# Performance work log

Measured on AMD Instinct MI355X. Metric: run time of the kernel, lower is better.

The kernel has to match this reference:

```python
import jax, jax.numpy as jnp
import numpy as np

SPLIT_PARAM = [4, 4, 4, 4]   # split sizes along h; sum == H
EPS = 1e-6                   # GeM clamp epsilon
NUM_SEGMENTS = 32            # number of packed sequences (B)


def setup_inputs() -> dict:
    key = jax.random.key(0)
    k1, k2 = jax.random.split(key)
    B, S, C, O, H, Wd = NUM_SEGMENTS, 4096, 128, 256, 16, 11
    x = jax.random.normal(k1, (1, C, S, H, Wd), dtype=jnp.float32)
    # ragged lengths: B positive ints summing exactly to S
    rng = np.random.default_rng(0)
    cuts = np.sort(rng.choice(np.arange(1, S), B - 1, replace=False))
    seqL = jnp.asarray(np.diff(np.concatenate([[0], cuts, [S]])), dtype=jnp.int32)
    W = jax.random.normal(k2, (O, C), dtype=jnp.float32) * 0.05  # 1x1 conv weight, bias=False
    p = jnp.ones((len(SPLIT_PARAM),), dtype=jnp.float32) * 6.5   # per-part GeM power
    return {"x": x, "seqL": seqL, "W": W, "p": p}


def reference(x, seqL, W, p):
    # x: [1, C, S, H, W] frames packed along dim 2; seqL: [B] lengths, sum == S
    _, C, S, H, Wd = x.shape
    # map each frame to its sequence id (ragged segment boundaries)
    bounds = jnp.cumsum(seqL)
    seg_ids = jnp.searchsorted(bounds, jnp.arange(S), side='right')  # [S]
    xs = jnp.transpose(x[0], (1, 0, 2, 3))                           # [S, C, H, W]
    pooled = jax.ops.segment_max(xs, seg_ids, num_segments=NUM_SEGMENTS)  # [B, C, H, W]
    # BasicConv2d: 1x1 conv, stride 1, no padding, no bias
    y = jnp.einsum('bchw,oc->bohw', pooled, W)                       # [B, O, H, W]
    # split along h and apply GeM (bin_num=[1]) with per-part power p[i]
    feats = []
    start = 0
    for i, sp in enumerate(SPLIT_PARAM):
        part = y[:, :, start:start + sp, :].reshape(y.shape[0], y.shape[1], -1)  # [B, O, sp*W]
        g = jnp.mean(jnp.clip(part, EPS, None) ** p[i], axis=-1) ** (1.0 / p[i])  # [B, O]
        feats.append(g[..., None])
        start += sp
    return jnp.concatenate(feats, -1)  # [B, O, m]
```

## Files before the change

kernel.cpp:

```cpp
#include <hip/hip_runtime.h>
#include <cmath>

#define C_DIM 128
#define S_DIM 4096
#define HW    176
#define B_SEG 32
#define O_DIM 256

__global__ __launch_bounds__(192) void seg_max_kernel(
    const float* __restrict__ x, const int* __restrict__ seqL,
    float* __restrict__ pooled)
{
    int bc = blockIdx.x;
    int c  = bc & (C_DIM - 1);
    int b  = bc >> 7;

    int s0 = 0;
    for (int i = 0; i < b; ++i) s0 += seqL[i];
    int len = seqL[b];

    int e = threadIdx.x;
    if (e >= HW) return;

    const float* xp = x + ((size_t)c * S_DIM + s0) * HW + e;
    float m = -INFINITY;
    int s = 0;
    for (; s + 4 <= len; s += 4) {
        float a0 = xp[(size_t)(s + 0) * HW];
        float a1 = xp[(size_t)(s + 1) * HW];
        float a2 = xp[(size_t)(s + 2) * HW];
        float a3 = xp[(size_t)(s + 3) * HW];
        m = fmaxf(m, fmaxf(fmaxf(a0, a1), fmaxf(a2, a3)));
    }
    for (; s < len; ++s) m = fmaxf(m, xp[(size_t)s * HW]);

    pooled[((size_t)b * C_DIM + c) * HW + e] = m;
}

__global__ __launch_bounds__(128) void conv_gem_kernel(
    const float* __restrict__ pooled, const float* __restrict__ Wm,
    const float* __restrict__ p, float* __restrict__ out)
{
    int bx = blockIdx.x;
    int b  = bx >> 3;
    int ot = bx & 7;
    int t  = threadIdx.x;
    int o_l  = t & 31;
    int part = t >> 5;
    int o = ot * 32 + o_l;

    __shared__ __align__(16) float pl[32 * HW];
    __shared__ float wl[32 * 33];

    float acc[44];
#pragma unroll
    for (int j = 0; j < 44; ++j) acc[j] = 0.f;

    for (int c0 = 0; c0 < C_DIM; c0 += 32) {
        __syncthreads();
        const float* src = pooled + ((size_t)b * C_DIM + c0) * HW;
        for (int i = t; i < 32 * HW; i += 128) pl[i] = src[i];
        for (int i = t; i < 32 * 32; i += 128) {
            int oo = i >> 5;
            int cc = i & 31;
            wl[cc * 33 + oo] = Wm[(size_t)(ot * 32 + oo) * C_DIM + c0 + cc];
        }
        __syncthreads();

        float wreg[32];
#pragma unroll
        for (int cc = 0; cc < 32; ++cc) wreg[cc] = wl[cc * 33 + o_l];

#pragma unroll 4
        for (int cc = 0; cc < 32; ++cc) {
            const float4* p4 = (const float4*)(pl + cc * HW + part * 44);
            float w = wreg[cc];
#pragma unroll
            for (int j = 0; j < 11; ++j) {
                float4 v = p4[j];
                acc[4 * j + 0] = fmaf(v.x, w, acc[4 * j + 0]);
                acc[4 * j + 1] = fmaf(v.y, w, acc[4 * j + 1]);
                acc[4 * j + 2] = fmaf(v.z, w, acc[4 * j + 2]);
                acc[4 * j + 3] = fmaf(v.w, w, acc[4 * j + 3]);
            }
        }
    }

    float pw = p[part];
    float s = 0.f;
#pragma unroll
    for (int j = 0; j < 44; ++j) {
        float v = fmaxf(acc[j], 1e-6f);
        s += __expf(pw * __logf(v));
    }
    float g = __powf(s * (1.0f / 44.0f), 1.0f / pw);
    out[((size_t)b * O_DIM + o) * 4 + part] = g;
}

extern "C" void kernel_launch(void* const* d_in, const int* in_sizes, int n_in,
                              void* d_out, int out_size, void* d_ws, size_t ws_size,
                              hipStream_t stream)
{
    const float* x    = (const float*)d_in[0];
    const int*   seqL = (const int*)d_in[1];
    const float* Wm   = (const float*)d_in[2];
    const float* p    = (const float*)d_in[3];
    float* out    = (float*)d_out;
    float* pooled = (float*)d_ws;

    seg_max_kernel<<<B_SEG * C_DIM, 192, 0, stream>>>(x, seqL, pooled);
    conv_gem_kernel<<<256, 128, 0, stream>>>(pooled, Wm, p, out);
}
```

Before: 555.0 us.

## Parallelize segment max across 8 wavefronts with float4 loads and shared reduction

The segment-max kernel now runs 512 threads per block: 8 wavefronts each take every 8th frame, 44 lanes per wavefront read float4 vectors, and partial maxima are combined through shared memory. The segment lengths are first staged in shared memory. The goal is more memory-level parallelism and wider loads on a bandwidth-bound 370MB read, at the cost of idle lanes (20 of 64 per wavefront) and an extra block-level sync and reduction.

```diff
diff --git a/kernel.cpp b/kernel.cpp
--- a/kernel.cpp
+++ b/kernel.cpp
@@ -4,10 +4,11 @@
 #define C_DIM 128
 #define S_DIM 4096
 #define HW    176
+#define HW4   44
 #define B_SEG 32
 #define O_DIM 256
 
-__global__ __launch_bounds__(192) void seg_max_kernel(
+__global__ __launch_bounds__(512) void seg_max_kernel(
     const float* __restrict__ x, const int* __restrict__ seqL,
     float* __restrict__ pooled)
 {
@@ -15,26 +16,52 @@
     int c  = bc & (C_DIM - 1);
     int b  = bc >> 7;
 
+    __shared__ int sL[B_SEG];
+    __shared__ __align__(16) float red[8][HW];
+
+    int t = threadIdx.x;
+    if (t < B_SEG) sL[t] = seqL[t];
+    __syncthreads();
+
     int s0 = 0;
-    for (int i = 0; i < b; ++i) s0 += seqL[i];
-    int len = seqL[b];
+    for (int i = 0; i < b; ++i) s0 += sL[i];
+    int len = sL[b];
 
-    int e = threadIdx.x;
-    if (e >= HW) return;
+    int w    = t >> 6;
+    int lane = t & 63;
 
-    const float* xp = x + ((size_t)c * S_DIM + s0) * HW + e;
-    float m = -INFINITY;
-    int s = 0;
-    for (; s + 4 <= len; s += 4) {
-        float a0 = xp[(size_t)(s + 0) * HW];
-        float a1 = xp[(size_t)(s + 1) * HW];
-        float a2 = xp[(size_t)(s + 2) * HW];
-        float a3 = xp[(size_t)(s + 3) * HW];
-        m = fmaxf(m, fmaxf(fmaxf(a0, a1), fmaxf(a2, a3)));
+    float4 m = make_float4(-INFINITY, -INFINITY, -INFINITY, -INFINITY);
+
+    if (lane < HW4) {
+        const float4* xp = (const float4*)(x + ((size_t)c * S_DIM + s0) * HW);
+        int s = w;
+        for (; s + 24 < len; s += 32) {
+            float4 a0 = xp[(size_t)(s     ) * HW4 + lane];
+            float4 a1 = xp[(size_t)(s +  8) * HW4 + lane];
+            float4 a2 = xp[(size_t)(s + 16) * HW4 + lane];
+            float4 a3 = xp[(size_t)(s + 24) * HW4 + lane];
+            m.x = fmaxf(m.x, fmaxf(fmaxf(a0.x, a1.x), fmaxf(a2.x, a3.x)));
+            m.y = fmaxf(m.y, fmaxf(fmaxf(a0.y, a1.y), fmaxf(a2.y, a3.y)));
+            m.z = fmaxf(m.z, fmaxf(fmaxf(a0.z, a1.z), fmaxf(a2.z, a3.z)));
+            m.w = fmaxf(m.w, fmaxf(fmaxf(a0.w, a1.w), fmaxf(a2.w, a3.w)));
+        }
+        for (; s < len; s += 8) {
+            float4 a = xp[(size_t)s * HW4 + lane];
+            m.x = fmaxf(m.x, a.x);
+            m.y = fmaxf(m.y, a.y);
+            m.z = fmaxf(m.z, a.z);
+            m.w = fmaxf(m.w, a.w);
+        }
+        ((float4*)red[w])[lane] = m;
     }
-    for (; s < len; ++s) m = fmaxf(m, xp[(size_t)s * HW]);
+    __syncthreads();
 
-    pooled[((size_t)b * C_DIM + c) * HW + e] = m;
+    if (t < HW) {
+        float r = red[0][t];
+#pragma unroll
+        for (int ww = 1; ww < 8; ++ww) r = fmaxf(r, red[ww][t]);
+        pooled[((size_t)b * C_DIM + c) * HW + t] = r;
+    }
 }
 
 __global__ __launch_bounds__(128) void conv_gem_kernel(
@@ -108,6 +135,6 @@
     float* out    = (float*)d_out;
     float* pooled = (float*)d_ws;
 
-    seg_max_kernel<<<B_SEG * C_DIM, 192, 0, stream>>>(x, seqL, pooled);
+    seg_max_kernel<<<B_SEG * C_DIM, 512, 0, stream>>>(x, seqL, pooled);
     conv_gem_kernel<<<256, 128, 0, stream>>>(pooled, Wm, p, out);
 }
```

Result: no change. 547.7 us (-1.3%).
